# Kernel tuning notes

Hardware: AMD Instinct MI355X
Metric: run time of the kernel (lower is better)

## Reference

```python
import jax, jax.numpy as jnp
import numpy as np

BITS = 4
IN_F = 4096
OUT_F = 4096
NUMVALS = 200000
TOPX = 10
B, S = 4, 2048


def setup_inputs() -> dict:
    key = jax.random.key(0)
    ks = jax.random.split(key, 9)
    x = jax.random.normal(ks[0], (B, S, IN_F), dtype=jnp.float32)
    qweight = jax.random.randint(ks[1], (IN_F // 32 * BITS, OUT_F),
                                 jnp.iinfo(jnp.int32).min, jnp.iinfo(jnp.int32).max,
                                 dtype=jnp.int32)
    lookup_table = jax.random.normal(ks[2], (OUT_F, 2 ** BITS), dtype=jnp.float32) * 0.02
    bias = jax.random.normal(ks[3], (OUT_F,), dtype=jnp.float32) * 0.01
    rows = jnp.sort(jax.random.randint(ks[4], (OUT_F + 1,), 0, NUMVALS, dtype=jnp.int32))
    rows = rows.at[0].set(0).at[-1].set(NUMVALS)  # valid CSR row pointers
    cols = jax.random.randint(ks[5], (NUMVALS,), 0, IN_F, dtype=jnp.int32)
    vals = jax.random.normal(ks[6], (NUMVALS,), dtype=jnp.float32) * 0.02
    full_rows = jax.random.normal(ks[7], (IN_F, TOPX), dtype=jnp.float32) * 0.02
    full_row_indices = (jnp.arange(TOPX, dtype=jnp.int32) * (OUT_F // TOPX))
    return {"x": x, "qweight": qweight, "lookup_table": lookup_table, "bias": bias,
            "rows": rows, "cols": cols, "vals": vals,
            "full_rows": full_rows, "full_row_indices": full_row_indices}


def _dequant(qweight, lookup_table):
    # unpack 4-bit codes packed along infeatures into each int32 word
    per_word = 32 // BITS
    shifts = (jnp.arange(per_word, dtype=jnp.int32) * BITS)
    codes = (qweight[:, None, :] >> shifts[None, :, None]) & ((1 << BITS) - 1)
    codes = codes.reshape(-1, qweight.shape[1])  # (IN_F, OUT_F)
    # per-output-channel LUT gather: W[i, j] = lut[j, codes[i, j]]
    return jnp.take_along_axis(lookup_table.T, codes, axis=0)  # (IN_F, OUT_F)


def reference(x, qweight, lookup_table, bias, rows, cols, vals, full_rows, full_row_indices):
    w = _dequant(qweight, lookup_table)  # (IN_F, OUT_F) float32
    # CSR sparse outlier correction (row pointers over output channels)
    nnz = vals.shape[0]
    row_ids = jnp.searchsorted(rows, jnp.arange(nnz, dtype=jnp.int32), side="right") - 1
    w = w.at[cols, row_ids].add(vals)
    # topX dense outlier channels
    w = w.at[:, full_row_indices].add(full_rows)
    tokens = x.reshape(-1, x.shape[-1])  # (B*S, IN_F)
    y = tokens @ w + bias
    return y.reshape(x.shape[:-1] + (w.shape[1],))
```

## Files before the change

kernel.cpp:

```cpp
#include <hip/hip_runtime.h>
#include <hip/hip_bf16.h>
#include <stdint.h>

#define IN_F 4096
#define OUT_F 4096
#define MTOK 8192
#define TOPX_N 10
#define NUMVALS 200000
#define CSR_BLOCKS ((NUMVALS + 255) / 256)
#define CVT_BLOCKS ((MTOK * IN_F / 8) / 256)

typedef __bf16 bf16x8 __attribute__((ext_vector_type(8)));
typedef float f32x4 __attribute__((ext_vector_type(4)));

__device__ __forceinline__ void gld_lds16(const void* g, void* l) {
    __builtin_amdgcn_global_load_lds((const __attribute__((address_space(1))) void*)g,
                                     (__attribute__((address_space(3))) void*)l, 16, 0, 0);
}

__global__ __launch_bounds__(256) void k_dequant(const int* __restrict__ qw,
                                                 const float* __restrict__ lut,
                                                 __bf16* __restrict__ Wt) {
    __shared__ int qs[64 * 65];
    __shared__ float ls[64 * 16];
    const int b = blockIdx.x;
    const int jc = (b & 63) * 64;
    const int wc = (b >> 6) * 64;
    const int t = threadIdx.x;

    {
        float4 v = *(const float4*)(lut + (size_t)(jc + (t >> 2)) * 16 + (t & 3) * 4);
        *(float4*)(ls + (t >> 2) * 16 + (t & 3) * 4) = v;
    }
#pragma unroll
    for (int p = 0; p < 4; ++p) {
        int idx = t + p * 256;
        int row = idx >> 4;
        int c4 = (idx & 15) * 4;
        int4 v = *(const int4*)(qw + (size_t)(wc + row) * OUT_F + jc + c4);
        int base = row * 65 + c4;
        qs[base] = v.x; qs[base + 1] = v.y; qs[base + 2] = v.z; qs[base + 3] = v.w;
    }
    __syncthreads();

    const int wave = t >> 6, lane = t & 63;
#pragma unroll
    for (int i = 0; i < 16; ++i) {
        const int c = wave * 16 + i;
        const unsigned q = (unsigned)qs[lane * 65 + c];
        const float* lp = ls + c * 16;
        bf16x8 v;
#pragma unroll
        for (int e = 0; e < 8; ++e) v[e] = (__bf16)lp[(q >> (4 * e)) & 15];
        *(bf16x8*)(Wt + (size_t)(jc + c) * IN_F + (size_t)(wc + lane) * 8) = v;
    }
}

__device__ __forceinline__ void bf16_cas_add(__bf16* Wt, size_t elem, float v) {
    unsigned* wp = (unsigned*)Wt + (elem >> 1);
    unsigned sh = (unsigned)(elem & 1) * 16;
    unsigned old = *wp, assumed;
    do {
        assumed = old;
        union { unsigned u; float f; } cv;
        cv.u = ((assumed >> sh) & 0xFFFFu) << 16;
        __bf16 nb = (__bf16)(cv.f + v);
        unsigned nh = *(unsigned short*)&nb;
        unsigned newv = (assumed & ~(0xFFFFu << sh)) | ((unsigned)nh << sh);
        old = atomicCAS(wp, assumed, newv);
    } while (old != assumed);
}

__global__ __launch_bounds__(256) void k_prep(const float* __restrict__ x,
                                              __bf16* __restrict__ xb,
                                              const int* __restrict__ rows,
                                              const int* __restrict__ cols,
                                              const float* __restrict__ vals,
                                              const float* __restrict__ fr,
                                              const int* __restrict__ fri,
                                              __bf16* __restrict__ Wt) {
    const int b = blockIdx.x;
    if (b < CVT_BLOCKS) {
        size_t t = (size_t)b * 256 + threadIdx.x;
        const float4* p = (const float4*)x + 2 * t;
        float4 a = p[0], c = p[1];
        bf16x8 v;
        v[0] = (__bf16)a.x; v[1] = (__bf16)a.y; v[2] = (__bf16)a.z; v[3] = (__bf16)a.w;
        v[4] = (__bf16)c.x; v[5] = (__bf16)c.y; v[6] = (__bf16)c.z; v[7] = (__bf16)c.w;
        ((bf16x8*)xb)[t] = v;
    } else if (b < CVT_BLOCKS + CSR_BLOCKS) {
        int n = (b - CVT_BLOCKS) * 256 + threadIdx.x;
        if (n >= NUMVALS) return;
        int lo = 0, hi = OUT_F + 1;
        while (lo < hi) {
            int mid = (lo + hi) >> 1;
            if (rows[mid] <= n) lo = mid + 1; else hi = mid;
        }
        int r = lo - 1;
        bf16_cas_add(Wt, (size_t)r * IN_F + cols[n], vals[n]);
    } else {
        int i = (b - CVT_BLOCKS - CSR_BLOCKS) * 256 + threadIdx.x;
        if (i >= IN_F) return;
#pragma unroll
        for (int t = 0; t < TOPX_N; ++t) {
            int j = fri[t];
            bf16_cas_add(Wt, (size_t)j * IN_F + i, fr[(size_t)i * TOPX_N + t]);
        }
    }
}

#define BK_G 32
#define NKT (IN_F / BK_G)
#define TILE_BYTES 16384
#define MFMA_ __builtin_amdgcn_mfma_f32_16x16x32_bf16

__global__ __launch_bounds__(512, 2) void k_gemm(const __bf16* __restrict__ A,
                                                 const __bf16* __restrict__ Bt,
                                                 const float* __restrict__ bias,
                                                 float* __restrict__ C) {
    __shared__ __align__(1024) char smem[3][2][TILE_BYTES];

    const int tid = threadIdx.x;
    const int wave = tid >> 6, lane = tid & 63;
    const int wm = wave >> 2, wn = wave & 3;

    const int bid = blockIdx.x;
    const int swz = (bid & 7) * 64 + (bid >> 3);
    const int n0 = (swz & 15) * 256;
    const int m0 = (swz >> 4) * 256;

    const int q = lane & 7, g = (lane >> 3) & 3, rh = lane >> 5;
    const int rloc = ((5 * (q - g + 8)) & 7) + 8 * rh;
    const int w0 = wave * 2;

    const char* gA0 = (const char*)(A  + (size_t)(m0 + w0 * 16 + rloc) * IN_F) + g * 16;
    const char* gA1 = gA0 + 16 * IN_F * 2;
    const char* gB0 = (const char*)(Bt + (size_t)(n0 + w0 * 16 + rloc) * IN_F) + g * 16;
    const char* gB1 = gB0 + 16 * IN_F * 2;
    char* lA = (char*)smem[0][0] + w0 * 1024;
    char* lB = (char*)smem[0][1] + w0 * 1024;

    const int lrow = lane & 15, kk = lane >> 4;
    const int rdc = ((5 * lrow + kk) & 7) * 16 + kk * 128 + (lrow >> 3) * 512;
    const int rdA = wm * 8192 + rdc;
    const int rdB = wn * 4096 + rdc;

#define STAGE(boff, koff) do {                               \
        gld_lds16(gA0 + (koff), lA + (boff));                \
        gld_lds16(gA1 + (koff), lA + (boff) + 1024);         \
        gld_lds16(gB0 + (koff), lB + (boff));                \
        gld_lds16(gB1 + (koff), lB + (boff) + 1024);         \
    } while (0)

#define COMPUTE(boff) do {                                                                     \
        const char* pA = (const char*)smem[0][0] + (boff) + rdA;                               \
        const char* pB = (const char*)smem[0][1] + (boff) + rdB;                               \
        bf16x8 bfr[4], af0[4], af1[4];                                                         \
        _Pragma("unroll") for (int n = 0; n < 4; ++n) bfr[n] = *(const bf16x8*)(pB + n * 1024);\
        _Pragma("unroll") for (int m = 0; m < 4; ++m) af0[m] = *(const bf16x8*)(pA + m * 1024);\
        _Pragma("unroll") for (int m = 0; m < 4; ++m) af1[m] = *(const bf16x8*)(pA + 4096 + m * 1024);\
        __builtin_amdgcn_s_setprio(1);                                                         \
        _Pragma("unroll") for (int m = 0; m < 4; ++m)                                          \
            _Pragma("unroll") for (int n = 0; n < 4; ++n)                                      \
                acc[m][n] = MFMA_(af0[m], bfr[n], acc[m][n], 0, 0, 0);                         \
        _Pragma("unroll") for (int m = 0; m < 4; ++m)                                          \
            _Pragma("unroll") for (int n = 0; n < 4; ++n)                                      \
                acc[m + 4][n] = MFMA_(af1[m], bfr[n], acc[m + 4][n], 0, 0, 0);                 \
        __builtin_amdgcn_s_setprio(0);                                                         \
    } while (0)

    f32x4 acc[8][4] = {};

    STAGE(0, 0);
    STAGE(32768, 64);

    int cboff = 0, sboff = 65536;
    for (int t = 0; t < NKT - 1; ++t) {
        asm volatile("s_waitcnt vmcnt(4)" ::: "memory");
        __builtin_amdgcn_s_barrier();
        asm volatile("" ::: "memory");
        if (t + 2 < NKT) STAGE(sboff, (t + 2) * 64);
        COMPUTE(cboff);
        cboff = cboff == 65536 ? 0 : cboff + 32768;
        sboff = sboff == 65536 ? 0 : sboff + 32768;
    }
    asm volatile("s_waitcnt vmcnt(0)" ::: "memory");
    __builtin_amdgcn_s_barrier();
    asm volatile("" ::: "memory");
    COMPUTE(cboff);

    const int m0w = m0 + wm * 128;
    const int n0w = n0 + wn * 64;
#pragma unroll
    for (int n = 0; n < 4; ++n) {
        const int col = n0w + n * 16 + lrow;
        const float bj = bias[col];
#pragma unroll
        for (int m = 0; m < 8; ++m) {
            const int row = m0w + m * 16 + kk * 4;
#pragma unroll
            for (int r = 0; r < 4; ++r)
                C[(size_t)(row + r) * OUT_F + col] = acc[m][n][r] + bj;
        }
    }
#undef STAGE
#undef COMPUTE
}

extern "C" void kernel_launch(void* const* d_in, const int* in_sizes, int n_in,
                              void* d_out, int out_size, void* d_ws, size_t ws_size,
                              hipStream_t stream) {
    const float* x         = (const float*)d_in[0];
    const int*   qweight   = (const int*)d_in[1];
    const float* lut       = (const float*)d_in[2];
    const float* bias      = (const float*)d_in[3];
    const int*   rows      = (const int*)d_in[4];
    const int*   cols      = (const int*)d_in[5];
    const float* vals      = (const float*)d_in[6];
    const float* full_rows = (const float*)d_in[7];
    const int*   fri       = (const int*)d_in[8];
    float* out = (float*)d_out;

    __bf16* Wt = (__bf16*)d_ws;
    __bf16* xb = (__bf16*)((char*)d_ws + (size_t)OUT_F * IN_F * 2);

    k_dequant<<<dim3(64 * 8), 256, 0, stream>>>(qweight, lut, Wt);
    k_prep<<<dim3(CVT_BLOCKS + CSR_BLOCKS + IN_F / 256), 256, 0, stream>>>(
        x, xb, rows, cols, vals, full_rows, fri, Wt);
    k_gemm<<<dim3((OUT_F / 256) * (MTOK / 256)), 512, 0, stream>>>(xb, Wt, bias, out);
}
```

Before: 530.9 us.

## Restructure GEMM main loop into 8-wave ping-pong schedule with BK=64 double buffering

```diff
diff --git a/kernel.cpp b/kernel.cpp
--- a/kernel.cpp
+++ b/kernel.cpp
@@ -109,85 +109,109 @@
     }
 }
 
-#define BK_G 32
-#define NKT (IN_F / BK_G)
-#define TILE_BYTES 16384
+#define BK_G 64
+#define ROWB (IN_F * 2)
+#define HB   ((size_t)128 * ROWB)
 #define MFMA_ __builtin_amdgcn_mfma_f32_16x16x32_bf16
+
+#define LGKM0 asm volatile("s_waitcnt lgkmcnt(0)")
+#define LGKM8 asm volatile("s_waitcnt lgkmcnt(8)")
+#define BAR   __builtin_amdgcn_s_barrier()
+#define VMC4  asm volatile("s_waitcnt vmcnt(4)" ::: "memory")
+#define VMC0  asm volatile("s_waitcnt vmcnt(0)" ::: "memory")
+#define MEMF  asm volatile("" ::: "memory")
+#define PRIO1 __builtin_amdgcn_s_setprio(1)
+#define PRIO0 __builtin_amdgcn_s_setprio(0)
 
 __global__ __launch_bounds__(512, 2) void k_gemm(const __bf16* __restrict__ A,
                                                  const __bf16* __restrict__ Bt,
                                                  const float* __restrict__ bias,
                                                  float* __restrict__ C) {
-    __shared__ __align__(1024) char smem[3][2][TILE_BYTES];
+    __shared__ __align__(1024) char smem[2][2][32768];
+    char* const sm = (char*)smem;
 
     const int tid = threadIdx.x;
-    const int wave = tid >> 6, lane = tid & 63;
-    const int wm = wave >> 2, wn = wave & 3;
+    const int wv = tid >> 6, l = tid & 63;
+    const int wm = wv >> 2, wn = wv & 3;
 
     const int bid = blockIdx.x;
     const int swz = (bid & 7) * 64 + (bid >> 3);
     const int n0 = (swz & 15) * 256;
     const int m0 = (swz >> 4) * 256;
 
-    const int q = lane & 7, g = (lane >> 3) & 3, rh = lane >> 5;
-    const int rloc = ((5 * (q - g + 8)) & 7) + 8 * rh;
-    const int w0 = wave * 2;
-
-    const char* gA0 = (const char*)(A  + (size_t)(m0 + w0 * 16 + rloc) * IN_F) + g * 16;
-    const char* gA1 = gA0 + 16 * IN_F * 2;
-    const char* gB0 = (const char*)(Bt + (size_t)(n0 + w0 * 16 + rloc) * IN_F) + g * 16;
-    const char* gB1 = gB0 + 16 * IN_F * 2;
-    char* lA = (char*)smem[0][0] + w0 * 1024;
-    char* lB = (char*)smem[0][1] + w0 * 1024;
-
-    const int lrow = lane & 15, kk = lane >> 4;
-    const int rdc = ((5 * lrow + kk) & 7) * 16 + kk * 128 + (lrow >> 3) * 512;
-    const int rdA = wm * 8192 + rdc;
-    const int rdB = wn * 4096 + rdc;
-
-#define STAGE(boff, koff) do {                               \
-        gld_lds16(gA0 + (koff), lA + (boff));                \
-        gld_lds16(gA1 + (koff), lA + (boff) + 1024);         \
-        gld_lds16(gB0 + (koff), lB + (boff));                \
-        gld_lds16(gB1 + (koff), lB + (boff) + 1024);         \
+    const int g = l >> 3;
+    const int rloc = ((l & 7) - g) & 7;
+    const int ld0 = wv * 1024 + l * 16;
+    const char* pa = (const char*)A  + (size_t)(m0 + wv * 8 + rloc) * ROWB + g * 16;
+    const char* pb = (const char*)Bt + (size_t)(n0 + wv * 8 + rloc) * ROWB + g * 16;
+
+#define STG(srcp, dstoff) do {                                    \
+        gld_lds16((srcp), sm + (dstoff) + ld0);                   \
+        gld_lds16((srcp) + 64 * ROWB, sm + (dstoff) + ld0 + 8192);\
     } while (0)
 
-#define COMPUTE(boff) do {                                                                     \
-        const char* pA = (const char*)smem[0][0] + (boff) + rdA;                               \
-        const char* pB = (const char*)smem[0][1] + (boff) + rdB;                               \
-        bf16x8 bfr[4], af0[4], af1[4];                                                         \
-        _Pragma("unroll") for (int n = 0; n < 4; ++n) bfr[n] = *(const bf16x8*)(pB + n * 1024);\
-        _Pragma("unroll") for (int m = 0; m < 4; ++m) af0[m] = *(const bf16x8*)(pA + m * 1024);\
-        _Pragma("unroll") for (int m = 0; m < 4; ++m) af1[m] = *(const bf16x8*)(pA + 4096 + m * 1024);\
-        __builtin_amdgcn_s_setprio(1);                                                         \
-        _Pragma("unroll") for (int m = 0; m < 4; ++m)                                          \
-            _Pragma("unroll") for (int n = 0; n < 4; ++n)                                      \
-                acc[m][n] = MFMA_(af0[m], bfr[n], acc[m][n], 0, 0, 0);                         \
-        _Pragma("unroll") for (int m = 0; m < 4; ++m)                                          \
-            _Pragma("unroll") for (int n = 0; n < 4; ++n)                                      \
-                acc[m + 4][n] = MFMA_(af1[m], bfr[n], acc[m + 4][n], 0, 0, 0);                 \
-        __builtin_amdgcn_s_setprio(0);                                                         \
-    } while (0)
+    const int lrow = l & 15, kk = l >> 4;
+    const int rd0 = (lrow >> 3) * 1024 + ((((lrow & 7) + kk) & 7)) * 16 + kk * 128;
+    const int rd1 = (lrow >> 3) * 1024 + ((((lrow & 7) + kk + 4) & 7)) * 16 + (kk + 4) * 128;
+    const int baA = wm * 16384;
+    const int baB = 32768 + wn * 8192;
 
     f32x4 acc[8][4] = {};
-
-    STAGE(0, 0);
-    STAGE(32768, 64);
-
-    int cboff = 0, sboff = 65536;
-    for (int t = 0; t < NKT - 1; ++t) {
-        asm volatile("s_waitcnt vmcnt(4)" ::: "memory");
-        __builtin_amdgcn_s_barrier();
-        asm volatile("" ::: "memory");
-        if (t + 2 < NKT) STAGE(sboff, (t + 2) * 64);
-        COMPUTE(cboff);
-        cboff = cboff == 65536 ? 0 : cboff + 32768;
-        sboff = sboff == 65536 ? 0 : sboff + 32768;
-    }
-    asm volatile("s_waitcnt vmcnt(0)" ::: "memory");
-    __builtin_amdgcn_s_barrier();
-    asm volatile("" ::: "memory");
-    COMPUTE(cboff);
+    bf16x8 af[4][2], bfr[4][2];
+
+#define RD_B(buf, nlo) do { _Pragma("unroll") for (int n_ = 0; n_ < 2; ++n_) {          \
+        bfr[(nlo) + n_][0] = *(const bf16x8*)(sm + (buf) + baB + ((nlo) + n_) * 2048 + rd0); \
+        bfr[(nlo) + n_][1] = *(const bf16x8*)(sm + (buf) + baB + ((nlo) + n_) * 2048 + rd1); } } while (0)
+#define RD_A(buf, mlo) do { _Pragma("unroll") for (int m_ = 0; m_ < 4; ++m_) {          \
+        af[m_][0] = *(const bf16x8*)(sm + (buf) + baA + ((mlo) + m_) * 2048 + rd0);     \
+        af[m_][1] = *(const bf16x8*)(sm + (buf) + baA + ((mlo) + m_) * 2048 + rd1); } } while (0)
+#define MFMA_Q(MB, NB) do { _Pragma("unroll") for (int m_ = 0; m_ < 4; ++m_)            \
+        _Pragma("unroll") for (int n_ = 0; n_ < 2; ++n_) {                              \
+            acc[(MB) + m_][(NB) + n_] = MFMA_(af[m_][0], bfr[(NB) + n_][0], acc[(MB) + m_][(NB) + n_], 0, 0, 0); \
+            acc[(MB) + m_][(NB) + n_] = MFMA_(af[m_][1], bfr[(NB) + n_][1], acc[(MB) + m_][(NB) + n_], 0, 0, 0); } } while (0)
+
+    STG(pb, 32768); STG(pb + HB, 49152);
+    STG(pa, 0);     STG(pa + HB, 16384);
+    STG(pb + 128, 98304); STG(pb + 128 + HB, 114688);
+    VMC4; BAR; MEMF;
+
+    for (int i = 0; i < 32; ++i) {
+        const bool stg = (i < 31);
+        RD_B(0, 0); RD_A(0, 0);
+        STG(pa + 128, 65536);
+        LGKM8; BAR; LGKM0;
+        PRIO1; MFMA_Q(0, 0); PRIO0; BAR;
+        RD_B(0, 2);
+        STG(pa + 128 + HB, 81920);
+        BAR; LGKM0;
+        PRIO1; MFMA_Q(0, 2); PRIO0; BAR;
+        RD_A(0, 4);
+        if (stg) STG(pb + 256, 32768);
+        BAR; LGKM0;
+        PRIO1; MFMA_Q(4, 2); PRIO0; BAR;
+        if (stg) STG(pb + 256 + HB, 49152);
+        BAR;
+        PRIO1; MFMA_Q(4, 0); PRIO0;
+        if (stg) { VMC4; } else { VMC0; }
+        BAR; MEMF;
+        RD_B(65536, 0); RD_A(65536, 0);
+        if (stg) STG(pa + 256, 0);
+        LGKM8; BAR; LGKM0;
+        PRIO1; MFMA_Q(0, 0); PRIO0; BAR;
+        RD_B(65536, 2);
+        if (stg) STG(pa + 256 + HB, 16384);
+        BAR; LGKM0;
+        PRIO1; MFMA_Q(0, 2); PRIO0; BAR;
+        RD_A(65536, 4);
+        if (stg) STG(pb + 384, 98304);
+        BAR; LGKM0;
+        PRIO1; MFMA_Q(4, 2); PRIO0; BAR;
+        if (stg) STG(pb + 384 + HB, 114688);
+        BAR;
+        PRIO1; MFMA_Q(4, 0); PRIO0;
+        if (stg) { VMC4; BAR; MEMF; }
+        pa += 256; pb += 256;
+    }
 
     const int m0w = m0 + wm * 128;
     const int n0w = n0 + wn * 64;
@@ -203,8 +227,10 @@
                 C[(size_t)(row + r) * OUT_F + col] = acc[m][n][r] + bj;
         }
     }
-#undef STAGE
-#undef COMPUTE
+#undef STG
+#undef RD_A
+#undef RD_B
+#undef MFMA_Q
 }
 
 extern "C" void kernel_launch(void* const* d_in, const int* in_sizes, int n_in,
```

Result: faster. 515.3 us (-2.9%).

## Shrink GEMM tile to 128x256 for higher occupancy; nontemporal x loads

Applied to the files above, without the earlier changes.

```diff
diff --git a/kernel.cpp b/kernel.cpp
--- a/kernel.cpp
+++ b/kernel.cpp
@@ -12,6 +12,7 @@
 
 typedef __bf16 bf16x8 __attribute__((ext_vector_type(8)));
 typedef float f32x4 __attribute__((ext_vector_type(4)));
+typedef float fvec4 __attribute__((ext_vector_type(4)));
 
 __device__ __forceinline__ void gld_lds16(const void* g, void* l) {
     __builtin_amdgcn_global_load_lds((const __attribute__((address_space(1))) void*)g,
@@ -82,11 +83,12 @@
     const int b = blockIdx.x;
     if (b < CVT_BLOCKS) {
         size_t t = (size_t)b * 256 + threadIdx.x;
-        const float4* p = (const float4*)x + 2 * t;
-        float4 a = p[0], c = p[1];
+        const fvec4* p = (const fvec4*)x + 2 * t;
+        fvec4 a = __builtin_nontemporal_load(p);
+        fvec4 c = __builtin_nontemporal_load(p + 1);
         bf16x8 v;
-        v[0] = (__bf16)a.x; v[1] = (__bf16)a.y; v[2] = (__bf16)a.z; v[3] = (__bf16)a.w;
-        v[4] = (__bf16)c.x; v[5] = (__bf16)c.y; v[6] = (__bf16)c.z; v[7] = (__bf16)c.w;
+        v[0] = (__bf16)a[0]; v[1] = (__bf16)a[1]; v[2] = (__bf16)a[2]; v[3] = (__bf16)a[3];
+        v[4] = (__bf16)c[0]; v[5] = (__bf16)c[1]; v[6] = (__bf16)c[2]; v[7] = (__bf16)c[3];
         ((bf16x8*)xb)[t] = v;
     } else if (b < CVT_BLOCKS + CSR_BLOCKS) {
         int n = (b - CVT_BLOCKS) * 256 + threadIdx.x;
@@ -111,92 +113,87 @@
 
 #define BK_G 32
 #define NKT (IN_F / BK_G)
-#define TILE_BYTES 16384
+#define ROWB (IN_F * 2)
+#define BUFB 24576
 #define MFMA_ __builtin_amdgcn_mfma_f32_16x16x32_bf16
-
-__global__ __launch_bounds__(512, 2) void k_gemm(const __bf16* __restrict__ A,
+#define ROT3(x) ((x) == 2 * BUFB ? 0 : (x) + BUFB)
+
+__global__ __launch_bounds__(512, 4) void k_gemm(const __bf16* __restrict__ A,
                                                  const __bf16* __restrict__ Bt,
                                                  const float* __restrict__ bias,
                                                  float* __restrict__ C) {
-    __shared__ __align__(1024) char smem[3][2][TILE_BYTES];
+    __shared__ __align__(1024) char smem[3 * BUFB];
+    char* const sm = smem;
 
     const int tid = threadIdx.x;
-    const int wave = tid >> 6, lane = tid & 63;
-    const int wm = wave >> 2, wn = wave & 3;
+    const int wv = tid >> 6, lane = tid & 63;
+    const int wm = wv >> 2, wn = wv & 3;
 
     const int bid = blockIdx.x;
-    const int swz = (bid & 7) * 64 + (bid >> 3);
+    const int swz = (bid & 7) * 128 + (bid >> 3);
     const int n0 = (swz & 15) * 256;
-    const int m0 = (swz >> 4) * 256;
+    const int m0 = (swz >> 4) * 128;
 
     const int q = lane & 7, g = (lane >> 3) & 3, rh = lane >> 5;
     const int rloc = ((5 * (q - g + 8)) & 7) + 8 * rh;
-    const int w0 = wave * 2;
-
-    const char* gA0 = (const char*)(A  + (size_t)(m0 + w0 * 16 + rloc) * IN_F) + g * 16;
-    const char* gA1 = gA0 + 16 * IN_F * 2;
-    const char* gB0 = (const char*)(Bt + (size_t)(n0 + w0 * 16 + rloc) * IN_F) + g * 16;
-    const char* gB1 = gB0 + 16 * IN_F * 2;
-    char* lA = (char*)smem[0][0] + w0 * 1024;
-    char* lB = (char*)smem[0][1] + w0 * 1024;
+
+    const char* gA  = (const char*)A  + (size_t)(m0 + wv * 16 + rloc) * ROWB + g * 16;
+    const char* gB  = (const char*)Bt + (size_t)(n0 + wv * 32 + rloc) * ROWB + g * 16;
+    const char* gB2 = gB + 16 * ROWB;
+    char* lA = sm + wv * 1024 + lane * 16;
+    char* lB = sm + 8192 + wv * 2048 + lane * 16;
+
+#define STAGE(boff, koff) do {                       \
+        gld_lds16(gA  + (koff), lA + (boff));        \
+        gld_lds16(gB  + (koff), lB + (boff));        \
+        gld_lds16(gB2 + (koff), lB + (boff) + 1024); \
+    } while (0)
 
     const int lrow = lane & 15, kk = lane >> 4;
     const int rdc = ((5 * lrow + kk) & 7) * 16 + kk * 128 + (lrow >> 3) * 512;
-    const int rdA = wm * 8192 + rdc;
-    const int rdB = wn * 4096 + rdc;
-
-#define STAGE(boff, koff) do {                               \
-        gld_lds16(gA0 + (koff), lA + (boff));                \
-        gld_lds16(gA1 + (koff), lA + (boff) + 1024);         \
-        gld_lds16(gB0 + (koff), lB + (boff));                \
-        gld_lds16(gB1 + (koff), lB + (boff) + 1024);         \
+    const int rdA = wm * 4096 + rdc;
+    const int rdB = 8192 + wn * 4096 + rdc;
+
+#define COMPUTE(boff) do {                                                        \
+        const char* pA = sm + (boff) + rdA;                                       \
+        const char* pB = sm + (boff) + rdB;                                       \
+        bf16x8 af[4], bfr[4];                                                     \
+        _Pragma("unroll") for (int n = 0; n < 4; ++n)                             \
+            bfr[n] = *(const bf16x8*)(pB + n * 1024);                             \
+        _Pragma("unroll") for (int m = 0; m < 4; ++m)                             \
+            af[m] = *(const bf16x8*)(pA + m * 1024);                              \
+        __builtin_amdgcn_s_setprio(1);                                            \
+        _Pragma("unroll") for (int m = 0; m < 4; ++m)                             \
+            _Pragma("unroll") for (int n = 0; n < 4; ++n)                         \
+                acc[m][n] = MFMA_(af[m], bfr[n], acc[m][n], 0, 0, 0);             \
+        __builtin_amdgcn_s_setprio(0);                                            \
     } while (0)
 
-#define COMPUTE(boff) do {                                                                     \
-        const char* pA = (const char*)smem[0][0] + (boff) + rdA;                               \
-        const char* pB = (const char*)smem[0][1] + (boff) + rdB;                               \
-        bf16x8 bfr[4], af0[4], af1[4];                                                         \
-        _Pragma("unroll") for (int n = 0; n < 4; ++n) bfr[n] = *(const bf16x8*)(pB + n * 1024);\
-        _Pragma("unroll") for (int m = 0; m < 4; ++m) af0[m] = *(const bf16x8*)(pA + m * 1024);\
-        _Pragma("unroll") for (int m = 0; m < 4; ++m) af1[m] = *(const bf16x8*)(pA + 4096 + m * 1024);\
-        __builtin_amdgcn_s_setprio(1);                                                         \
-        _Pragma("unroll") for (int m = 0; m < 4; ++m)                                          \
-            _Pragma("unroll") for (int n = 0; n < 4; ++n)                                      \
-                acc[m][n] = MFMA_(af0[m], bfr[n], acc[m][n], 0, 0, 0);                         \
-        _Pragma("unroll") for (int m = 0; m < 4; ++m)                                          \
-            _Pragma("unroll") for (int n = 0; n < 4; ++n)                                      \
-                acc[m + 4][n] = MFMA_(af1[m], bfr[n], acc[m + 4][n], 0, 0, 0);                 \
-        __builtin_amdgcn_s_setprio(0);                                                         \
-    } while (0)
-
-    f32x4 acc[8][4] = {};
+    f32x4 acc[4][4] = {};
 
     STAGE(0, 0);
-    STAGE(32768, 64);
-
-    int cboff = 0, sboff = 65536;
-    for (int t = 0; t < NKT - 1; ++t) {
-        asm volatile("s_waitcnt vmcnt(4)" ::: "memory");
+    STAGE(BUFB, 64);
+
+    int cboff = 0, sboff = 2 * BUFB;
+    for (int t = 0; t < NKT; ++t) {
+        if (t < NKT - 1) { asm volatile("s_waitcnt vmcnt(3)" ::: "memory"); }
+        else             { asm volatile("s_waitcnt vmcnt(0)" ::: "memory"); }
         __builtin_amdgcn_s_barrier();
         asm volatile("" ::: "memory");
         if (t + 2 < NKT) STAGE(sboff, (t + 2) * 64);
         COMPUTE(cboff);
-        cboff = cboff == 65536 ? 0 : cboff + 32768;
-        sboff = sboff == 65536 ? 0 : sboff + 32768;
-    }
-    asm volatile("s_waitcnt vmcnt(0)" ::: "memory");
-    __builtin_amdgcn_s_barrier();
-    asm volatile("" ::: "memory");
-    COMPUTE(cboff);
-
-    const int m0w = m0 + wm * 128;
+        cboff = ROT3(cboff);
+        sboff = ROT3(sboff);
+    }
+
+    const int m0w = m0 + wm * 64;
     const int n0w = n0 + wn * 64;
 #pragma unroll
     for (int n = 0; n < 4; ++n) {
         const int col = n0w + n * 16 + lrow;
         const float bj = bias[col];
 #pragma unroll
-        for (int m = 0; m < 8; ++m) {
+        for (int m = 0; m < 4; ++m) {
             const int row = m0w + m * 16 + kk * 4;
 #pragma unroll
             for (int r = 0; r < 4; ++r)
@@ -227,5 +224,5 @@
     k_dequant<<<dim3(64 * 8), 256, 0, stream>>>(qweight, lut, Wt);
     k_prep<<<dim3(CVT_BLOCKS + CSR_BLOCKS + IN_F / 256), 256, 0, stream>>>(
         x, xb, rows, cols, vals, full_rows, fri, Wt);
-    k_gemm<<<dim3((OUT_F / 256) * (MTOK / 256)), 512, 0, stream>>>(xb, Wt, bias, out);
-}
+    k_gemm<<<dim3((OUT_F / 256) * (MTOK / 128)), 512, 0, stream>>>(xb, Wt, bias, out);
+}
```

After: 611.7 us. 15.2% more time.
